# Optimization experiments

Hardware: AMD Instinct MI355X
Metric: run time of the kernel (lower is better)

Reference implementation:

```python
import jax, jax.numpy as jnp
import numpy as np
from jax import lax

B, T, U, V, D, H = 4, 256, 64, 1024, 256, 256
BLANK = V - 1
NEG = -1.0e30
CTC_W = 0.3


def setup_inputs():
    ks = jax.random.split(jax.random.key(0), 9)
    return {
        "x_enc": jax.random.normal(ks[0], (B, T, D), jnp.float32),
        "x_dec": jax.random.normal(ks[1], (B, U + 1, H), jnp.float32),
        "W_enc": jax.random.normal(ks[2], (D, H), jnp.float32) / float(np.sqrt(D)),
        "b_enc": jnp.zeros((H,), jnp.float32),
        "W_dec": jax.random.normal(ks[3], (H, H), jnp.float32) / float(np.sqrt(H)),
        "b_dec": jnp.zeros((H,), jnp.float32),
        "W_out": jax.random.normal(ks[4], (H, V), jnp.float32) / float(np.sqrt(H)),
        "b_out": jnp.zeros((V,), jnp.float32),
        "W_ctc": jax.random.normal(ks[5], (D, V), jnp.float32) / float(np.sqrt(D)),
        "b_ctc": jnp.zeros((V,), jnp.float32),
        "target": jax.random.randint(ks[6], (B, U), 0, V - 1, jnp.int32),
        "frame_length": (T - jax.random.randint(ks[7], (B,), 0, T // 4)).astype(jnp.int32),
        "target_length": (U - jax.random.randint(ks[8], (B,), 0, U // 4)).astype(jnp.int32),
    }


def _forward(x_enc, x_dec, W_enc, b_enc, W_dec, b_dec, W_out, b_out, W_ctc, b_ctc,
             target, frame_length, target_length):
    b_idx = jnp.arange(B)
    ft, tl = frame_length, target_length

    # ---- Joiner: broadcast-add of projected enc/pred states, tanh, output proj ----
    h = jnp.tanh((x_enc @ W_enc + b_enc)[:, :, None, :]
                 + (x_dec @ W_dec + b_dec)[:, None, :, :])        # [B,T,U+1,H]
    logp = jax.nn.log_softmax(h @ W_out + b_out, axis=-1)          # [B,T,U+1,V]

    # gather=True trick: only blank and target-label log-probs are needed
    lp_blank = logp[..., BLANK]                                    # [B,T,U+1]
    lp_label = jnp.take_along_axis(
        logp[:, :, :U, :],
        jnp.broadcast_to(target[:, None, :, None], (B, T, U, 1)), axis=3)[..., 0]  # [B,T,U]

    # ---- RNNT forward DP over the (T, U+1) lattice ----
    def u_scan(b0, lbl):
        # b0[u] = alpha[t-1,u] + blank[t-1,u]; alpha[t,u] = logaddexp(b0[u], alpha[t,u-1]+lbl[u-1])
        def step(c, xs):
            bu, lu = xs
            new = jnp.logaddexp(bu, c + lu)
            return new, new
        _, outs = lax.scan(step, b0[:, 0],
                           (jnp.moveaxis(b0[:, 1:], 1, 0), jnp.moveaxis(lbl, 1, 0)))
        return jnp.concatenate([b0[:, :1], jnp.moveaxis(outs, 0, 1)], axis=1)

    alpha0 = jnp.concatenate([jnp.zeros((B, 1), logp.dtype),
                              jnp.cumsum(lp_label[:, 0, :], axis=1)], axis=1)  # [B,U+1]

    def t_step(prev, xs):
        blk_prev, lbl_t = xs
        a = u_scan(prev + blk_prev, lbl_t)
        return a, a

    _, rest = lax.scan(t_step, alpha0,
                       (jnp.moveaxis(lp_blank[:, :-1, :], 1, 0),
                        jnp.moveaxis(lp_label[:, 1:, :], 1, 0)))
    alphas = jnp.concatenate([alpha0[None], rest], axis=0)          # [T,B,U+1]
    ll = alphas[ft - 1, b_idx, tl] + lp_blank[b_idx, ft - 1, tl]
    rnnt_loss = jnp.mean(-ll)

    # ---- CTC branch: linear head on encoder output + standard CTC DP ----
    logp_ctc = jax.nn.log_softmax(x_enc @ W_ctc + b_ctc, axis=-1)   # [B,T,V]
    S = 2 * U + 1
    ext = jnp.full((B, S), BLANK, jnp.int32).at[:, 1::2].set(target)
    emit = jnp.take_along_axis(logp_ctc,
                               jnp.broadcast_to(ext[:, None, :], (B, T, S)), axis=2)  # [B,T,S]
    skip = jnp.concatenate([jnp.zeros((B, 2), bool),
                            (ext[:, 2:] != BLANK) & (ext[:, 2:] != ext[:, :-2])], axis=1)
    c0 = jnp.full((B, S), NEG, logp_ctc.dtype).at[:, 0].set(emit[:, 0, 0]).at[:, 1].set(emit[:, 0, 1])

    def c_step(prev, xs):
        emit_t, t = xs
        p2 = jnp.concatenate([jnp.full((B, 1), NEG, prev.dtype), prev[:, :-1]], axis=1)
        p3 = jnp.where(skip,
                       jnp.concatenate([jnp.full((B, 2), NEG, prev.dtype), prev[:, :-2]], axis=1),
                       NEG)
        new = emit_t + jnp.logaddexp(jnp.logaddexp(prev, p2), p3)
        new = jnp.where((t < ft)[:, None], new, prev)  # freeze past frame_length
        return new, None

    cT, _ = lax.scan(c_step, c0, (jnp.moveaxis(emit[:, 1:, :], 1, 0), jnp.arange(1, T)))
    s_last = 2 * tl
    ll_ctc = jnp.logaddexp(cT[b_idx, s_last], cT[b_idx, s_last - 1])
    ctc_loss = jnp.where(ll_ctc < NEG / 2, 0.0, -ll_ctc).sum() / B  # zero_infinity, sum/B

    return rnnt_loss + CTC_W * ctc_loss


def reference(x_enc, x_dec, W_enc, b_enc, W_dec, b_dec, W_out, b_out, W_ctc, b_ctc,
              target, frame_length, target_length):
    return _forward(x_enc, x_dec, W_enc, b_enc, W_dec, b_dec, W_out, b_out, W_ctc, b_ctc,
                    target, frame_length, target_length)
```

## Files before the change

### kernel.cpp

```cpp
#include <hip/hip_runtime.h>
#include <hip/hip_bf16.h>

#define Bn 4
#define Tn 256
#define Un 64
#define UP1 65
#define Vn 1024
#define Dn 256
#define Hn 256
#define BLANKC 1023
#define NEGF (-1.0e30f)
#define CTCW 0.3f
#define R2E 1.4426950408889634f
#define LN2 0.6931471805599453f

typedef __attribute__((ext_vector_type(8))) short short8;
typedef __attribute__((ext_vector_type(4))) float f32x4;
typedef __attribute__((ext_vector_type(4))) unsigned int u32x4;

static __device__ __forceinline__ unsigned short f2bf(float f) {
  unsigned int u = __float_as_uint(f);
  u += 0x7FFFu + ((u >> 16) & 1u);
  return (unsigned short)(u >> 16);
}
static __device__ __forceinline__ unsigned int pack2bf(float a, float b) {
  return (unsigned int)f2bf(a) | ((unsigned int)f2bf(b) << 16);
}
static __device__ __forceinline__ float ftanh(float x) {
  float e = __expf(2.0f * x);
  return 1.0f - 2.0f / (e + 1.0f);
}
static __device__ __forceinline__ float ex2(float x) {
  return __builtin_amdgcn_exp2f(x);
}
static __device__ __forceinline__ float lg2(float x) {
  return __builtin_amdgcn_logf(x);
}
static __device__ __forceinline__ float laddexp2_(float x, float y) {
  float m = fmaxf(x, y);
  float d = y - x;
  return m + lg2(1.0f + ex2(-fabsf(d)));
}
static __device__ __forceinline__ float laddexp3_2(float a, float b, float c) {
  float m = fmaxf(fmaxf(a, b), c);
  return m + lg2(ex2(a - m) + ex2(b - m) + ex2(c - m));
}
static __device__ __forceinline__ float shfl_up1(float x) {
  int r = __builtin_amdgcn_update_dpp(0, __float_as_int(x), 0x138, 0xF, 0xF, false);
  return __int_as_float(r);
}

__global__ __launch_bounds__(256) void k_prep(
    const float* __restrict__ W_enc, const float* __restrict__ W_dec,
    const float* __restrict__ W_out, const float* __restrict__ W_ctc,
    unsigned short* __restrict__ Wt_enc, unsigned short* __restrict__ Wt_dec,
    unsigned short* __restrict__ Wt_out, unsigned short* __restrict__ Wt_ctc,
    float* __restrict__ out) {
  const int blk = blockIdx.x, tid = threadIdx.x;
  if (blk == 0 && tid == 0) out[0] = 0.0f;
  __shared__ float tilebuf[64][65];
  if (blk < 128) {
    const float* Wsrc = (blk < 64) ? W_out : W_ctc;
    unsigned short* Wd = (blk < 64) ? Wt_out : Wt_ctc;
    const int tt = blk & 63;
    const int k0 = (tt & 3) * 64, v0 = (tt >> 2) * 64;
#pragma unroll
    for (int rep = 0; rep < 16; ++rep) {
      int e = rep * 256 + tid;
      int rr = e >> 6, cc = e & 63;
      tilebuf[rr][cc] = Wsrc[(k0 + rr) * 1024 + (v0 + cc)];
    }
    __syncthreads();
#pragma unroll
    for (int rep = 0; rep < 16; ++rep) {
      int e = rep * 256 + tid;
      int nn = e >> 6, kk = e & 63;
      int n = v0 + nn, k = k0 + kk;
      int c = n >> 8, col = n & 255;
      int ks = k >> 5, sub = (k >> 3) & 3, k7 = k & 7;
      Wd[(c * 8 + ks) * 8192 + sub * 2048 + col * 8 + k7] = f2bf(tilebuf[kk][nn]);
    }
  } else {
    const float* Wsrc = (blk < 144) ? W_enc : W_dec;
    unsigned short* Wd = (blk < 144) ? Wt_enc : Wt_dec;
    const int tt = (blk - 128) & 15;
    const int k0 = (tt & 3) * 64, v0 = (tt >> 2) * 64;
#pragma unroll
    for (int rep = 0; rep < 16; ++rep) {
      int e = rep * 256 + tid;
      int rr = e >> 6, cc = e & 63;
      tilebuf[rr][cc] = Wsrc[(k0 + rr) * 256 + (v0 + cc)];
    }
    __syncthreads();
#pragma unroll
    for (int rep = 0; rep < 16; ++rep) {
      int e = rep * 256 + tid;
      int rr = e >> 6, cc = e & 63;
      Wd[(v0 + rr) * 256 + (k0 + cc)] = f2bf(tilebuf[cc][rr]);
    }
  }
}

__global__ __launch_bounds__(256) void k_lin(
    const float* __restrict__ x_enc, const float* __restrict__ x_dec,
    const unsigned short* __restrict__ Wt_enc, const float* __restrict__ b_enc,
    const unsigned short* __restrict__ Wt_dec, const float* __restrict__ b_dec,
    float* __restrict__ enc_lin, float* __restrict__ dec_lin) {
  __shared__ __align__(16) char Asw[32 * 512];
  const int tid = threadIdx.x;
  const int w = tid >> 6, l = tid & 63;
  const int l15 = l & 15, l4 = l >> 4;
  const bool enc = blockIdx.x < 32;
  const int m0 = enc ? blockIdx.x * 32 : (blockIdx.x - 32) * 32;
  const int Mlim = enc ? 1024 : 260;
  const float* xp = enc ? x_enc : x_dec;
  const unsigned short* Wt = enc ? Wt_enc : Wt_dec;
  const float* bias = enc ? b_enc : b_dec;
  float* outp = enc ? enc_lin : dec_lin;

#pragma unroll
  for (int it = 0; it < 4; ++it) {
    int e = (it << 8) + tid;
    int i = e >> 5;
    int k0 = (e & 31) << 3;
    int r = m0 + i;
    if (r > Mlim - 1) r = Mlim - 1;
    const float* sp = xp + r * 256 + k0;
    f32x4 e0 = *(const f32x4*)sp;
    f32x4 e1 = *(const f32x4*)(sp + 4);
    u32x4 pv;
    pv[0] = pack2bf(e0[0], e0[1]);
    pv[1] = pack2bf(e0[2], e0[3]);
    pv[2] = pack2bf(e1[0], e1[1]);
    pv[3] = pack2bf(e1[2], e1[3]);
    int byt = (i << 9) + (k0 << 1);
    byt ^= (i & 7) << 4;
    *(u32x4*)(Asw + byt) = pv;
  }
  __syncthreads();

  const int nb = w * 64;
  f32x4 acc[2][4] = {};
#pragma unroll
  for (int ks = 0; ks < 8; ++ks) {
    int k = ks * 32 + l4 * 8;
    short8 af[2];
#pragma unroll
    for (int mt = 0; mt < 2; ++mt) {
      int i = mt * 16 + l15;
      int byt = (i << 9) + (k << 1);
      byt ^= (i & 7) << 4;
      af[mt] = *(const short8*)(Asw + byt);
    }
    short8 bfr[4];
#pragma unroll
    for (int nt = 0; nt < 4; ++nt) {
      int n = nb + nt * 16 + l15;
      bfr[nt] = *(const short8*)(Wt + n * 256 + k);
    }
#pragma unroll
    for (int mt = 0; mt < 2; ++mt)
#pragma unroll
      for (int nt = 0; nt < 4; ++nt)
        acc[mt][nt] = __builtin_amdgcn_mfma_f32_16x16x32_bf16(
            af[mt], bfr[nt], acc[mt][nt], 0, 0, 0);
  }
  float biasv[4];
#pragma unroll
  for (int nt = 0; nt < 4; ++nt) biasv[nt] = bias[nb + nt * 16 + l15];
#pragma unroll
  for (int mt = 0; mt < 2; ++mt)
#pragma unroll
    for (int rr = 0; rr < 4; ++rr) {
      int row = m0 + mt * 16 + l4 * 4 + rr;
      if (row < Mlim) {
#pragma unroll
        for (int nt = 0; nt < 4; ++nt)
          outp[row * 256 + nb + nt * 16 + l15] = acc[mt][nt][rr] + biasv[nt];
      }
    }
}

__global__ __launch_bounds__(256) void k_join2(
    const float* __restrict__ enc_lin, const float* __restrict__ dec_lin,
    const unsigned short* __restrict__ Wt_out, const float* __restrict__ b_out,
    const float* __restrict__ x_enc,
    const unsigned short* __restrict__ Wt_ctc, const float* __restrict__ b_ctc,
    const int* __restrict__ target,
    float* __restrict__ lp_blank, float* __restrict__ lp_label,
    float* __restrict__ ctc_blank, float* __restrict__ ctc_lse,
    float* __restrict__ ctc_lab) {
  __shared__ __align__(16) char Asw[64 * 512];
  __shared__ float s_psum[4][64];
  __shared__ float s_blank[64], s_label[64];
  __shared__ int s_tgt[64];

  const int tid = threadIdx.x;
  const int w = tid >> 6, l = tid & 63;
  const int l15 = l & 15, l4 = l >> 4;
  const int bid = blockIdx.x;

  const bool joiner = bid >= 16;
  const unsigned short* Wt = joiner ? Wt_out : Wt_ctc;
  const float* bias = joiner ? b_out : b_ctc;

  const unsigned short* tb = Wt + l4 * 2048 + (w * 64 + l15) * 8;

  short8 bE[4], bO[4];
#define LOADB(REG, S)                                                          \
  {                                                                            \
    const unsigned short* p_ = tb + (S)*8192;                                  \
    _Pragma("unroll") for (int nt = 0; nt < 4; ++nt)                           \
        REG[nt] = *(const short8*)(p_ + nt * 128);                             \
  }
  {
    const int sc0 = (bid & 3) * 8;
    LOADB(bE, sc0 + 0)
    LOADB(bO, sc0 + 1)
  }

  int b, r0 = 0, g0 = 0;
  if (joiner) {
    const int jbid = bid - 16;
    b = jbid / 260;
    r0 = (jbid % 260) * 64;
#pragma unroll
    for (int it = 0; it < 8; ++it) {
      int e = (it << 8) + tid;
      int i = e >> 5;
      int k0 = (e & 31) << 3;
      int r = r0 + i;
      int t = r / 65;
      int u = r - t * 65;
      const float* ep = enc_lin + ((b * Tn + t) * Hn + k0);
      const float* dp = dec_lin + ((b * UP1 + u) * Hn + k0);
      f32x4 e0 = *(const f32x4*)ep;
      f32x4 e1 = *(const f32x4*)(ep + 4);
      f32x4 d0 = *(const f32x4*)dp;
      f32x4 d1 = *(const f32x4*)(dp + 4);
      u32x4 pv;
      pv[0] = pack2bf(ftanh(e0[0] + d0[0]) * R2E, ftanh(e0[1] + d0[1]) * R2E);
      pv[1] = pack2bf(ftanh(e0[2] + d0[2]) * R2E, ftanh(e0[3] + d0[3]) * R2E);
      pv[2] = pack2bf(ftanh(e1[0] + d1[0]) * R2E, ftanh(e1[1] + d1[1]) * R2E);
      pv[3] = pack2bf(ftanh(e1[2] + d1[2]) * R2E, ftanh(e1[3] + d1[3]) * R2E);
      int byt = (i << 9) + (k0 << 1);
      byt ^= (i & 7) << 4;
      *(u32x4*)(Asw + byt) = pv;
    }
    if (tid < 64) {
      int u = (r0 + tid) % 65;
      s_tgt[tid] = (u < Un) ? target[b * Un + u] : -1;
    }
  } else {
    g0 = bid * 64;
    b = g0 >> 8;
#pragma unroll
    for (int it = 0; it < 8; ++it) {
      int e = (it << 8) + tid;
      int i = e >> 5;
      int k0 = (e & 31) << 3;
      const float* sp = x_enc + (g0 + i) * Dn + k0;
      f32x4 e0 = *(const f32x4*)sp;
      f32x4 e1 = *(const f32x4*)(sp + 4);
      u32x4 pv;
      pv[0] = pack2bf(e0[0] * R2E, e0[1] * R2E);
      pv[1] = pack2bf(e0[2] * R2E, e0[3] * R2E);
      pv[2] = pack2bf(e1[0] * R2E, e1[1] * R2E);
      pv[3] = pack2bf(e1[2] * R2E, e1[3] * R2E);
      int byt = (i << 9) + (k0 << 1);
      byt ^= (i & 7) << 4;
      *(u32x4*)(Asw + byt) = pv;
    }
    if (tid < 64) s_tgt[tid] = target[b * Un + tid];
  }
  __syncthreads();

  float ssum[16];
#pragma unroll
  for (int j = 0; j < 16; ++j) ssum[j] = 0.0f;

#define MFMASTEP(REG, KS)                                                      \
  {                                                                            \
    __builtin_amdgcn_s_setprio(1);                                             \
    const int k_ = (KS)*32 + l4 * 8;                                           \
    _Pragma("unroll") for (int mt = 0; mt < 4; ++mt) {                         \
      int i_ = mt * 16 + l15;                                                  \
      int byt_ = ((i_ << 9) + (k_ << 1)) ^ ((i_ & 7) << 4);                    \
      short8 af_ = *(const short8*)(Asw + byt_);                               \
      _Pragma("unroll") for (int nt = 0; nt < 4; ++nt)                         \
          acc[mt][nt] = __builtin_amdgcn_mfma_f32_16x16x32_bf16(               \
              af_, REG[nt], acc[mt][nt], 0, 0, 0);                             \
    }                                                                          \
    __builtin_amdgcn_s_setprio(0);                                             \
  }
#define SB __builtin_amdgcn_sched_barrier(0)

#pragma unroll 1
  for (int cr = 0; cr < 4; ++cr) {
    const int cc = (cr + bid) & 3;
    const int sc = cc * 8;
    const int scn = ((cr + 1 + bid) & 3) * 8;
    f32x4 acc[4][4] = {};
    MFMASTEP(bE, 0) LOADB(bE, sc + 2) SB;
    MFMASTEP(bO, 1) LOADB(bO, sc + 3) SB;
    MFMASTEP(bE, 2) LOADB(bE, sc + 4) SB;
    MFMASTEP(bO, 3) LOADB(bO, sc + 5) SB;
    MFMASTEP(bE, 4) LOADB(bE, sc + 6) SB;
    MFMASTEP(bO, 5) LOADB(bO, sc + 7) SB;
    MFMASTEP(bE, 6) LOADB(bE, (cr < 3) ? scn + 0 : sc + 6) SB;
    MFMASTEP(bO, 7) LOADB(bO, (cr < 3) ? scn + 1 : sc + 7) SB;

    const int nb = cc * 256 + w * 64;
    float biasv[4];
#pragma unroll
    for (int nt = 0; nt < 4; ++nt) biasv[nt] = bias[nb + nt * 16 + l15] * R2E;
#pragma unroll
    for (int mt = 0; mt < 4; ++mt)
#pragma unroll
      for (int nt = 0; nt < 4; ++nt)
#pragma unroll
        for (int rr = 0; rr < 4; ++rr) acc[mt][nt][rr] += biasv[nt];

    if (joiner) {
      if (cc == 3 && w == 3 && l15 == 15) {
#pragma unroll
        for (int mt = 0; mt < 4; ++mt)
#pragma unroll
          for (int rr = 0; rr < 4; ++rr)
            s_blank[mt * 16 + l4 * 4 + rr] = acc[mt][3][rr];
      }
#pragma unroll
      for (int mt = 0; mt < 4; ++mt)
#pragma unroll
        for (int rr = 0; rr < 4; ++rr) {
          int row = mt * 16 + l4 * 4 + rr;
          int tg = s_tgt[row];
          if ((tg >> 8) == cc && ((tg >> 6) & 3) == w && (tg & 15) == l15) {
            int ntv = (tg >> 4) & 3;
            float v01 = (ntv & 1) ? acc[mt][1][rr] : acc[mt][0][rr];
            float v23 = (ntv & 1) ? acc[mt][3][rr] : acc[mt][2][rr];
            s_label[row] = (ntv & 2) ? v23 : v01;
          }
        }
    } else {
      if (cc == 3 && w == 3 && l15 == 15) {
#pragma unroll
        for (int mt = 0; mt < 4; ++mt)
#pragma unroll
          for (int rr = 0; rr < 4; ++rr)
            s_blank[mt * 16 + l4 * 4 + rr] = acc[mt][3][rr];
      }
#pragma unroll 1
      for (int u = 0; u < 64; ++u) {
        int tgu = s_tgt[u];
        if ((tgu >> 8) == cc && ((tgu >> 6) & 3) == w) {
          int ntv = (tgu >> 4) & 3;
          if ((tgu & 15) == l15) {
#pragma unroll
            for (int mt = 0; mt < 4; ++mt)
#pragma unroll
              for (int rr = 0; rr < 4; ++rr) {
                float v01 = (ntv & 1) ? acc[mt][1][rr] : acc[mt][0][rr];
                float v23 = (ntv & 1) ? acc[mt][3][rr] : acc[mt][2][rr];
                float v = (ntv & 2) ? v23 : v01;
                ctc_lab[(g0 + mt * 16 + l4 * 4 + rr) * 64 + u] = v;
              }
          }
        }
      }
    }
#pragma unroll
    for (int mt = 0; mt < 4; ++mt)
#pragma unroll
      for (int rr = 0; rr < 4; ++rr)
        ssum[mt * 4 + rr] += ex2(acc[mt][0][rr]) + ex2(acc[mt][1][rr]) +
                             ex2(acc[mt][2][rr]) + ex2(acc[mt][3][rr]);
  }
#undef MFMASTEP
#undef LOADB
#undef SB

#pragma unroll
  for (int ms = 1; ms < 16; ms <<= 1)
#pragma unroll
    for (int j = 0; j < 16; ++j) ssum[j] += __shfl_xor(ssum[j], ms, 64);
  if (l15 == 0) {
#pragma unroll
    for (int j = 0; j < 16; ++j)
      s_psum[w][(j >> 2) * 16 + l4 * 4 + (j & 3)] = ssum[j];
  }
  __syncthreads();

  if (tid < 64) {
    float tot = s_psum[0][tid] + s_psum[1][tid] + s_psum[2][tid] + s_psum[3][tid];
    float lse = lg2(tot);
    if (joiner) {
      int r = r0 + tid;
      int t = r / 65;
      int u = r - t * 65;
      lp_blank[(b * Tn + t) * UP1 + u] = s_blank[tid] - lse;
      if (u < Un) lp_label[(b * Tn + t) * Un + u] = s_label[tid] - lse;
    } else {
      ctc_blank[g0 + tid] = s_blank[tid] - lse;
      ctc_lse[g0 + tid] = lse;
    }
  }
}

__global__ __launch_bounds__(256) void k_dp(
    const float* __restrict__ lp_blank, const float* __restrict__ lp_label,
    const float* __restrict__ ctc_blank, const float* __restrict__ ctc_lse,
    const float* __restrict__ ctc_lab,
    const int* __restrict__ target,
    const int* __restrict__ flen, const int* __restrict__ tlen,
    float* __restrict__ out) {
  __shared__ float sA[256 * 66];
  __shared__ __align__(16) float sB[16384];
  __shared__ float sC[256], sD[256];
  __shared__ float cT[129];
  const int tid = threadIdx.x;
  const int l = tid & 63;

  if (blockIdx.x < 4) {
    const int b = blockIdx.x;
    for (int i = tid; i < 16640; i += 256) {
      int r = i / 65, cidx = i - r * 65;
      sA[r * 66 + cidx] = lp_blank[b * 16640 + i];
    }
    {
      const f32x4* g2 = (const f32x4*)(lp_label + b * 16384);
      f32x4* s2 = (f32x4*)sB;
      for (int i = tid; i < 4096; i += 256) s2[i] = g2[i];
    }
    __syncthreads();
    if (tid < 64) {
      const int ft = flen[b], tl = tlen[b];
      const int dstar = ft - 1 + tl;
      const bool isown = (l == tl);
      const bool is64 = (tl == 64) && (l == 63);
      const int lc = (l >= 1) ? l - 1 : 0;

#define RLOAD(D0, VB, VL, VB64, VL64)                                          \
  _Pragma("unroll") for (int j = 0; j < 8; ++j) {                              \
    const int d_ = (D0) + j;                                                   \
    const int t_ = d_ - l;                                                     \
    const int tbc_ = (t_ < 1) ? 1 : (t_ > 255 ? 255 : t_);                     \
    const int tcc_ = (t_ < 0) ? 0 : (t_ > 255 ? 255 : t_);                     \
    VB[j] = sA[(tbc_ - 1) * 66 + l];                                           \
    VL[j] = (l == 0) ? NEGF : sB[tcc_ * 64 + lc];                              \
    const int t64_ = d_ - 64;                                                  \
    const int t64b_ = (t64_ < 1) ? 1 : (t64_ > 255 ? 255 : t64_);              \
    const int t64c_ = (t64_ < 0) ? 0 : (t64_ > 255 ? 255 : t64_);              \
    VB64[j] = sA[(t64b_ - 1) * 66 + 64];                                       \
    VL64[j] = sB[t64c_ * 64 + 63];                                             \
  }

      float cvb[8], cvl[8], cvb64[8], cvl64[8];
      RLOAD(1, cvb, cvl, cvb64, cvl64);
      float a = (l == 0) ? 0.0f : NEGF;
      float a64 = NEGF, cap = NEGF;
      for (int d0 = 1; d0 <= dstar; d0 += 8) {
        float nvb[8], nvl[8], nvb64[8], nvl64[8];
        RLOAD(d0 + 8, nvb, nvl, nvb64, nvl64);
        __builtin_amdgcn_sched_barrier(0);
        const bool hashit = ((unsigned)(dstar - d0)) < 8u;
        if (hashit) {
#pragma unroll
          for (int j = 0; j < 8; ++j) {
            const int d = d0 + j;
            float aleft = shfl_up1(a);
            float x = a + cvb[j];
            float y = aleft + cvl[j];
            float nw = laddexp2_(x, y);
            float nw64 = laddexp2_(a64 + cvb64[j], a + cvl64[j]);
            a = nw;
            a64 = (l == 63) ? nw64 : a64;
            bool hit = (d == dstar);
            cap = (hit && isown) ? a : cap;
            cap = (hit && is64) ? a64 : cap;
          }
        } else {
#pragma unroll
          for (int j = 0; j < 8; ++j) {
            float aleft = shfl_up1(a);
            float x = a + cvb[j];
            float y = aleft + cvl[j];
            float nw = laddexp2_(x, y);
            float nw64 = laddexp2_(a64 + cvb64[j], a + cvl64[j]);
            a = nw;
            a64 = (l == 63) ? nw64 : a64;
          }
        }
        __builtin_amdgcn_sched_barrier(0);
#pragma unroll
        for (int j = 0; j < 8; ++j) {
          cvb[j] = nvb[j];
          cvl[j] = nvl[j];
          cvb64[j] = nvb64[j];
          cvl64[j] = nvl64[j];
        }
      }
#undef RLOAD
      bool owner = (tl < 64) ? isown : (l == 63);
      if (owner)
        atomicAdd(out, -0.25f * LN2 * (cap + sA[(ft - 1) * 66 + tl]));
    }
  } else {
    const int b = blockIdx.x - 4;
    {
      const f32x4* g2 = (const f32x4*)(ctc_lab + b * 16384);
      f32x4* s2 = (f32x4*)sB;
      for (int i = tid; i < 4096; i += 256) s2[i] = g2[i];
      sC[tid] = ctc_blank[b * 256 + tid];
      sD[tid] = ctc_lse[b * 256 + tid];
    }
    __syncthreads();
    if (tid < 64) {
      const int ft = flen[b], tl = tlen[b];
      const int tg = target[b * Un + l];
      const int tgp = (l >= 1) ? target[b * Un + l - 1] : -1;
      const bool skip1 = (l >= 1) && (tg != tgp);

#define CLOAD(T0, EB, E1)                                                      \
  _Pragma("unroll") for (int j = 0; j < 8; ++j) {                              \
    const int tc_ = ((T0) + j > 255) ? 255 : (T0) + j;                         \
    EB[j] = sC[tc_];                                                           \
    E1[j] = sB[tc_ * 64 + l] - sD[tc_];                                        \
  }

      float ceb[8], ce1[8];
      CLOAD(1, ceb, ce1);
      float a0 = (l == 0) ? sC[0] : NEGF;
      float a1 = (l == 0) ? (sB[0] - sD[0]) : NEGF;
      float a2 = NEGF;
      for (int t0 = 1; t0 < ft; t0 += 8) {
        float neb[8], ne1[8];
        CLOAD(t0 + 8, neb, ne1);
        __builtin_amdgcn_sched_barrier(0);
        const bool alive = (t0 + 8 <= ft);
        if (alive) {
#pragma unroll
          for (int j = 0; j < 8; ++j) {
            float pm1 = shfl_up1(a1);
            pm1 = (l == 0) ? NEGF : pm1;
            float n0 = ceb[j] + laddexp2_(a0, pm1);
            float n1 = ce1[j] + laddexp3_2(a1, a0, skip1 ? pm1 : NEGF);
            float n2 = ceb[j] + laddexp2_(a2, a1);
            a0 = n0;
            a1 = n1;
            a2 = (l == 63) ? n2 : a2;
          }
        } else {
#pragma unroll
          for (int j = 0; j < 8; ++j) {
            const int t = t0 + j;
            float pm1 = shfl_up1(a1);
            pm1 = (l == 0) ? NEGF : pm1;
            float n0 = ceb[j] + laddexp2_(a0, pm1);
            float n1 = ce1[j] + laddexp3_2(a1, a0, skip1 ? pm1 : NEGF);
            float n2 = ceb[j] + laddexp2_(a2, a1);
            bool run = (t < ft);
            a0 = run ? n0 : a0;
            a1 = run ? n1 : a1;
            a2 = (run && (l == 63)) ? n2 : a2;
          }
        }
        __builtin_amdgcn_sched_barrier(0);
#pragma unroll
        for (int j = 0; j < 8; ++j) {
          ceb[j] = neb[j];
          ce1[j] = ne1[j];
        }
      }
#undef CLOAD
      cT[2 * l] = a0;
      cT[2 * l + 1] = a1;
      if (l == 63) cT[128] = a2;
      __builtin_amdgcn_s_waitcnt(0);
      if (l == 0) {
        int sl = 2 * tl;
        float ll = laddexp2_(cT[sl], cT[sl - 1]);
        float lb = (ll < NEGF * 0.7f) ? 0.0f : -ll;
        atomicAdd(out, CTCW * 0.25f * LN2 * lb);
      }
    }
  }
}

extern "C" void kernel_launch(void* const* d_in, const int* in_sizes, int n_in,
                              void* d_out, int out_size, void* d_ws, size_t ws_size,
                              hipStream_t stream) {
  (void)in_sizes; (void)n_in; (void)out_size; (void)ws_size;
  const float* x_enc = (const float*)d_in[0];
  const float* x_dec = (const float*)d_in[1];
  const float* W_enc = (const float*)d_in[2];
  const float* b_enc = (const float*)d_in[3];
  const float* W_dec = (const float*)d_in[4];
  const float* b_dec = (const float*)d_in[5];
  const float* W_out = (const float*)d_in[6];
  const float* b_out = (const float*)d_in[7];
  const float* W_ctc = (const float*)d_in[8];
  const float* b_ctc = (const float*)d_in[9];
  const int* target = (const int*)d_in[10];
  const int* flen = (const int*)d_in[11];
  const int* tlen = (const int*)d_in[12];

  float* ws = (float*)d_ws;
  float* enc_lin = ws;
  float* dec_lin = ws + 262144;
  float* lp_blank = ws + 328704;
  float* lp_label = ws + 395264;
  float* ctc_blank = ws + 460800;
  float* ctc_lse = ws + 461824;
  float* ctc_lab = ws + 462848;
  unsigned short* Wt_out = (unsigned short*)(ws + 528384);
  unsigned short* Wt_ctc = Wt_out + 262144;
  unsigned short* Wt_enc = (unsigned short*)lp_blank;
  unsigned short* Wt_dec = (unsigned short*)lp_label;
  float* out = (float*)d_out;

  k_prep<<<dim3(160), dim3(256), 0, stream>>>(
      W_enc, W_dec, W_out, W_ctc, Wt_enc, Wt_dec, Wt_out, Wt_ctc, out);
  k_lin<<<dim3(41), dim3(256), 0, stream>>>(
      x_enc, x_dec, Wt_enc, b_enc, Wt_dec, b_dec, enc_lin, dec_lin);
  k_join2<<<dim3(1056), dim3(256), 0, stream>>>(
      enc_lin, dec_lin, Wt_out, b_out, x_enc, Wt_ctc, b_ctc, target,
      lp_blank, lp_label, ctc_blank, ctc_lse, ctc_lab);
  k_dp<<<dim3(8), dim3(64 * 4), 0, stream>>>(
      lp_blank, lp_label, ctc_blank, ctc_lse, ctc_lab, target, flen, tlen, out);
}
```

Measured before the change: 120.3 us.

## Fuse weight prep and enc/dec projection into one kernel, drop setprio

```diff
diff --git a/kernel.cpp b/kernel.cpp
--- a/kernel.cpp
+++ b/kernel.cpp
@@ -50,16 +50,21 @@
   return __int_as_float(r);
 }
 
-__global__ __launch_bounds__(256) void k_prep(
-    const float* __restrict__ W_enc, const float* __restrict__ W_dec,
+__global__ __launch_bounds__(256) void k_pre(
+    const float* __restrict__ x_enc, const float* __restrict__ x_dec,
+    const float* __restrict__ W_enc, const float* __restrict__ b_enc,
+    const float* __restrict__ W_dec, const float* __restrict__ b_dec,
     const float* __restrict__ W_out, const float* __restrict__ W_ctc,
-    unsigned short* __restrict__ Wt_enc, unsigned short* __restrict__ Wt_dec,
     unsigned short* __restrict__ Wt_out, unsigned short* __restrict__ Wt_ctc,
+    float* __restrict__ enc_lin, float* __restrict__ dec_lin,
     float* __restrict__ out) {
   const int blk = blockIdx.x, tid = threadIdx.x;
   if (blk == 0 && tid == 0) out[0] = 0.0f;
-  __shared__ float tilebuf[64][65];
+  const int w = tid >> 6, l = tid & 63;
+  const int l15 = l & 15, l4 = l >> 4;
+
   if (blk < 128) {
+    __shared__ float tilebuf[64][65];
     const float* Wsrc = (blk < 64) ? W_out : W_ctc;
     unsigned short* Wd = (blk < 64) ? Wt_out : Wt_ctc;
     const int tt = blk & 63;
@@ -81,104 +86,82 @@
       Wd[(c * 8 + ks) * 8192 + sub * 2048 + col * 8 + k7] = f2bf(tilebuf[kk][nn]);
     }
   } else {
-    const float* Wsrc = (blk < 144) ? W_enc : W_dec;
-    unsigned short* Wd = (blk < 144) ? Wt_enc : Wt_dec;
-    const int tt = (blk - 128) & 15;
-    const int k0 = (tt & 3) * 64, v0 = (tt >> 2) * 64;
-#pragma unroll
-    for (int rep = 0; rep < 16; ++rep) {
-      int e = rep * 256 + tid;
-      int rr = e >> 6, cc = e & 63;
-      tilebuf[rr][cc] = Wsrc[(k0 + rr) * 256 + (v0 + cc)];
+    __shared__ __align__(16) char Asw[32 * 512];
+    const int lb = blk - 128;
+    const bool enc = lb < 32;
+    const int m0 = enc ? lb * 32 : (lb - 32) * 32;
+    const int Mlim = enc ? 1024 : 260;
+    const float* xp = enc ? x_enc : x_dec;
+    const float* Wsrc = enc ? W_enc : W_dec;
+    const float* bias = enc ? b_enc : b_dec;
+    float* outp = enc ? enc_lin : dec_lin;
+
+#pragma unroll
+    for (int it = 0; it < 4; ++it) {
+      int e = (it << 8) + tid;
+      int i = e >> 5;
+      int k0 = (e & 31) << 3;
+      int r = m0 + i;
+      if (r > Mlim - 1) r = Mlim - 1;
+      const float* sp = xp + r * 256 + k0;
+      f32x4 e0 = *(const f32x4*)sp;
+      f32x4 e1 = *(const f32x4*)(sp + 4);
+      u32x4 pv;
+      pv[0] = pack2bf(e0[0], e0[1]);
+      pv[1] = pack2bf(e0[2], e0[3]);
+      pv[2] = pack2bf(e1[0], e1[1]);
+      pv[3] = pack2bf(e1[2], e1[3]);
+      int byt = (i << 9) + (k0 << 1);
+      byt ^= (i & 7) << 4;
+      *(u32x4*)(Asw + byt) = pv;
     }
     __syncthreads();
-#pragma unroll
-    for (int rep = 0; rep < 16; ++rep) {
-      int e = rep * 256 + tid;
-      int rr = e >> 6, cc = e & 63;
-      Wd[(v0 + rr) * 256 + (k0 + cc)] = f2bf(tilebuf[cc][rr]);
-    }
-  }
-}
-
-__global__ __launch_bounds__(256) void k_lin(
-    const float* __restrict__ x_enc, const float* __restrict__ x_dec,
-    const unsigned short* __restrict__ Wt_enc, const float* __restrict__ b_enc,
-    const unsigned short* __restrict__ Wt_dec, const float* __restrict__ b_dec,
-    float* __restrict__ enc_lin, float* __restrict__ dec_lin) {
-  __shared__ __align__(16) char Asw[32 * 512];
-  const int tid = threadIdx.x;
-  const int w = tid >> 6, l = tid & 63;
-  const int l15 = l & 15, l4 = l >> 4;
-  const bool enc = blockIdx.x < 32;
-  const int m0 = enc ? blockIdx.x * 32 : (blockIdx.x - 32) * 32;
-  const int Mlim = enc ? 1024 : 260;
-  const float* xp = enc ? x_enc : x_dec;
-  const unsigned short* Wt = enc ? Wt_enc : Wt_dec;
-  const float* bias = enc ? b_enc : b_dec;
-  float* outp = enc ? enc_lin : dec_lin;
-
-#pragma unroll
-  for (int it = 0; it < 4; ++it) {
-    int e = (it << 8) + tid;
-    int i = e >> 5;
-    int k0 = (e & 31) << 3;
-    int r = m0 + i;
-    if (r > Mlim - 1) r = Mlim - 1;
-    const float* sp = xp + r * 256 + k0;
-    f32x4 e0 = *(const f32x4*)sp;
-    f32x4 e1 = *(const f32x4*)(sp + 4);
-    u32x4 pv;
-    pv[0] = pack2bf(e0[0], e0[1]);
-    pv[1] = pack2bf(e0[2], e0[3]);
-    pv[2] = pack2bf(e1[0], e1[1]);
-    pv[3] = pack2bf(e1[2], e1[3]);
-    int byt = (i << 9) + (k0 << 1);
-    byt ^= (i & 7) << 4;
-    *(u32x4*)(Asw + byt) = pv;
-  }
-  __syncthreads();
-
-  const int nb = w * 64;
-  f32x4 acc[2][4] = {};
-#pragma unroll
-  for (int ks = 0; ks < 8; ++ks) {
-    int k = ks * 32 + l4 * 8;
-    short8 af[2];
-#pragma unroll
-    for (int mt = 0; mt < 2; ++mt) {
-      int i = mt * 16 + l15;
-      int byt = (i << 9) + (k << 1);
-      byt ^= (i & 7) << 4;
-      af[mt] = *(const short8*)(Asw + byt);
-    }
-    short8 bfr[4];
-#pragma unroll
-    for (int nt = 0; nt < 4; ++nt) {
-      int n = nb + nt * 16 + l15;
-      bfr[nt] = *(const short8*)(Wt + n * 256 + k);
-    }
+
+    const int nb = w * 64;
+    f32x4 acc[2][4] = {};
+#pragma unroll
+    for (int ks = 0; ks < 8; ++ks) {
+      int k = ks * 32 + l4 * 8;
+      short8 af[2];
+#pragma unroll
+      for (int mt = 0; mt < 2; ++mt) {
+        int i = mt * 16 + l15;
+        int byt = (i << 9) + (k << 1);
+        byt ^= (i & 7) << 4;
+        af[mt] = *(const short8*)(Asw + byt);
+      }
+      short8 bfr[4];
+#pragma unroll
+      for (int nt = 0; nt < 4; ++nt) {
+        int n = nb + nt * 16 + l15;
+        const float* wp = Wsrc + k * 256 + n;
+        short8 v;
+#pragma unroll
+        for (int j = 0; j < 8; ++j) v[j] = (short)f2bf(wp[j * 256]);
+        bfr[nt] = v;
+      }
+#pragma unroll
+      for (int mt = 0; mt < 2; ++mt)
+#pragma unroll
+        for (int nt = 0; nt < 4; ++nt)
+          acc[mt][nt] = __builtin_amdgcn_mfma_f32_16x16x32_bf16(
+              af[mt], bfr[nt], acc[mt][nt], 0, 0, 0);
+    }
+    float biasv[4];
+#pragma unroll
+    for (int nt = 0; nt < 4; ++nt) biasv[nt] = bias[nb + nt * 16 + l15];
 #pragma unroll
     for (int mt = 0; mt < 2; ++mt)
 #pragma unroll
-      for (int nt = 0; nt < 4; ++nt)
-        acc[mt][nt] = __builtin_amdgcn_mfma_f32_16x16x32_bf16(
-            af[mt], bfr[nt], acc[mt][nt], 0, 0, 0);
-  }
-  float biasv[4];
-#pragma unroll
-  for (int nt = 0; nt < 4; ++nt) biasv[nt] = bias[nb + nt * 16 + l15];
-#pragma unroll
-  for (int mt = 0; mt < 2; ++mt)
-#pragma unroll
-    for (int rr = 0; rr < 4; ++rr) {
-      int row = m0 + mt * 16 + l4 * 4 + rr;
-      if (row < Mlim) {
-#pragma unroll
-        for (int nt = 0; nt < 4; ++nt)
-          outp[row * 256 + nb + nt * 16 + l15] = acc[mt][nt][rr] + biasv[nt];
-      }
-    }
+      for (int rr = 0; rr < 4; ++rr) {
+        int row = m0 + mt * 16 + l4 * 4 + rr;
+        if (row < Mlim) {
+#pragma unroll
+          for (int nt = 0; nt < 4; ++nt)
+            outp[row * 256 + nb + nt * 16 + l15] = acc[mt][nt][rr] + biasv[nt];
+        }
+      }
+  }
 }
 
 __global__ __launch_bounds__(256) void k_join2(
@@ -281,7 +264,6 @@
 
 #define MFMASTEP(REG, KS)                                                      \
   {                                                                            \
-    __builtin_amdgcn_s_setprio(1);                                             \
     const int k_ = (KS)*32 + l4 * 8;                                           \
     _Pragma("unroll") for (int mt = 0; mt < 4; ++mt) {                         \
       int i_ = mt * 16 + l15;                                                  \
@@ -291,7 +273,6 @@
           acc[mt][nt] = __builtin_amdgcn_mfma_f32_16x16x32_bf16(               \
               af_, REG[nt], acc[mt][nt], 0, 0, 0);                             \
     }                                                                          \
-    __builtin_amdgcn_s_setprio(0);                                             \
   }
 #define SB __builtin_amdgcn_sched_barrier(0)
 
@@ -469,12 +450,9 @@
           for (int j = 0; j < 8; ++j) {
             const int d = d0 + j;
             float aleft = shfl_up1(a);
-            float x = a + cvb[j];
-            float y = aleft + cvl[j];
-            float nw = laddexp2_(x, y);
-            float nw64 = laddexp2_(a64 + cvb64[j], a + cvl64[j]);
+            float nw = laddexp2_(a + cvb[j], aleft + cvl[j]);
+            a64 = laddexp2_(a64 + cvb64[j], a + cvl64[j]);
             a = nw;
-            a64 = (l == 63) ? nw64 : a64;
             bool hit = (d == dstar);
             cap = (hit && isown) ? a : cap;
             cap = (hit && is64) ? a64 : cap;
@@ -483,12 +461,9 @@
 #pragma unroll
           for (int j = 0; j < 8; ++j) {
             float aleft = shfl_up1(a);
-            float x = a + cvb[j];
-            float y = aleft + cvl[j];
-            float nw = laddexp2_(x, y);
-            float nw64 = laddexp2_(a64 + cvb64[j], a + cvl64[j]);
+            float nw = laddexp2_(a + cvb[j], aleft + cvl[j]);
+            a64 = laddexp2_(a64 + cvb64[j], a + cvl64[j]);
             a = nw;
-            a64 = (l == 63) ? nw64 : a64;
           }
         }
         __builtin_amdgcn_sched_barrier(0);
@@ -545,10 +520,9 @@
             pm1 = (l == 0) ? NEGF : pm1;
             float n0 = ceb[j] + laddexp2_(a0, pm1);
             float n1 = ce1[j] + laddexp3_2(a1, a0, skip1 ? pm1 : NEGF);
-            float n2 = ceb[j] + laddexp2_(a2, a1);
+            a2 = ceb[j] + laddexp2_(a2, a1);
             a0 = n0;
             a1 = n1;
-            a2 = (l == 63) ? n2 : a2;
           }
         } else {
 #pragma unroll
@@ -562,7 +536,7 @@
             bool run = (t < ft);
             a0 = run ? n0 : a0;
             a1 = run ? n1 : a1;
-            a2 = (run && (l == 63)) ? n2 : a2;
+            a2 = run ? n2 : a2;
           }
         }
         __builtin_amdgcn_sched_barrier(0);
@@ -615,14 +589,11 @@
   float* ctc_lab = ws + 462848;
   unsigned short* Wt_out = (unsigned short*)(ws + 528384);
   unsigned short* Wt_ctc = Wt_out + 262144;
-  unsigned short* Wt_enc = (unsigned short*)lp_blank;
-  unsigned short* Wt_dec = (unsigned short*)lp_label;
   float* out = (float*)d_out;
 
-  k_prep<<<dim3(160), dim3(256), 0, stream>>>(
-      W_enc, W_dec, W_out, W_ctc, Wt_enc, Wt_dec, Wt_out, Wt_ctc, out);
-  k_lin<<<dim3(41), dim3(256), 0, stream>>>(
-      x_enc, x_dec, Wt_enc, b_enc, Wt_dec, b_dec, enc_lin, dec_lin);
+  k_pre<<<dim3(169), dim3(256), 0, stream>>>(
+      x_enc, x_dec, W_enc, b_enc, W_dec, b_dec, W_out, W_ctc,
+      Wt_out, Wt_ctc, enc_lin, dec_lin, out);
   k_join2<<<dim3(1056), dim3(256), 0, stream>>>(
       enc_lin, dec_lin, Wt_out, b_out, x_enc, Wt_ctc, b_ctc, target,
       lp_blank, lp_label, ctc_blank, ctc_lse, ctc_lab);
```

After: 113.7 us. 1.06x faster.
